# Optimization experiments

Measured on AMD Instinct MI355X. Metric: run time of the kernel, lower is better.

Reference implementation:

```python
import jax, jax.numpy as jnp
import numpy as np

B, T, D, H = 32, 2048, 512, 512


def setup_inputs() -> dict:
    key = jax.random.key(0)
    k1, k2 = jax.random.split(key)
    x = jax.random.normal(k1, (B, T, D), dtype=jnp.float32)
    # Linear(D+H -> 4H); xavier-uniform-ish init
    limit = float(np.sqrt(6.0 / ((D + H) + 4 * H)))
    W = jax.random.uniform(k2, (D + H, 4 * H), minval=-limit, maxval=limit, dtype=jnp.float32)
    b = jnp.zeros((4 * H,), dtype=jnp.float32)
    b = b.at[H:2 * H].set(1.0)  # forget-gate bias init = 1
    h0 = jnp.zeros((B, H), dtype=jnp.float32)
    c0 = jnp.zeros((B, H), dtype=jnp.float32)
    return {"x": x, "W": W, "b": b, "h0": h0, "c0": c0}


def reference(x, W, b, h0, c0):
    # Split weight into input and hidden parts to avoid per-step concat.
    Wx, Wh = W[:D], W[D:]  # (D,4H), (H,4H)
    # Precompute input projections for all timesteps: (T,B,4H)
    xg = jnp.einsum('btd,dg->tbg', x, Wx) + b

    def step(carry, xg_t):
        h, c = carry
        gates = xg_t + h @ Wh  # (B,4H)
        i, f, g, o = jnp.split(gates, 4, axis=-1)
        i = jax.nn.sigmoid(i)
        f = jax.nn.sigmoid(f)
        g = jnp.tanh(g)
        o = jax.nn.sigmoid(o)
        c_t = f * c + i * g
        h_t = o * jnp.tanh(c_t)
        return (h_t, c_t), h_t

    (h_T, c_T), hs = jax.lax.scan(step, (h0, c0), xg)  # hs: (T,B,H)
    outputs = jnp.transpose(hs, (1, 0, 2))  # (B,T,H)
    return outputs, (h_T, c_T)
```

## Files before the change

### kernel.cpp

```cpp
#include <hip/hip_runtime.h>

#define TT 2048
#define BB 32
#define DD 512
#define HH 512
#define NWG 64
#define NTHR 256

typedef short s8v __attribute__((ext_vector_type(8)));
typedef float f4v __attribute__((ext_vector_type(4)));
typedef unsigned u4v __attribute__((ext_vector_type(4)));
typedef unsigned long long u64;

union UF { u4v u; s8v s; };

__device__ __forceinline__ float asf(unsigned u) { return __uint_as_float(u); }

__device__ __forceinline__ unsigned cvtpk(float a, float b) {
    unsigned r;
    asm("v_cvt_pk_bf16_f32 %0, %1, %2" : "=v"(r) : "v"(a), "v"(b));
    return r;
}
__device__ __forceinline__ void split2(float a, float b, unsigned& hp, unsigned& lp) {
    hp = cvtpk(a, b);
    lp = cvtpk(a - asf(hp << 16), b - asf(hp & 0xFFFF0000u));
}

__global__ void lstm_init(const float* __restrict__ h0, const float* __restrict__ c0,
                          unsigned* __restrict__ hhi, float* __restrict__ cbuf,
                          unsigned* __restrict__ flags) {
    int j = blockIdx.x * blockDim.x + threadIdx.x;
    if (j < NWG * 4) flags[j] = 0u;
    if (j < BB * HH / 2) hhi[j] = cvtpk(h0[2 * j], h0[2 * j + 1]);
    cbuf[j] = c0[j];
}

__global__ __launch_bounds__(NTHR) void gemm_xg(
    const float* __restrict__ x, const float* __restrict__ W,
    const float* __restrict__ bias, float* __restrict__ xg, int t0)
{
    const int wg8 = blockIdx.x & 63;
    const int tcb = blockIdx.x >> 6;
    const int tid = threadIdx.x;
    const int u0  = wg8 * 8;
    const int wv  = tid >> 6, ln = tid & 63;
    const int bh  = wv >> 1, ch = wv & 1;
    const int fl  = ln & 15, fg = ln >> 4;

    s8v whi[16], wlo[16];
    const int col32 = ch * 16 + fl;
    const int gcol  = ((col32 >> 3) << 9) + u0 + (col32 & 7);
    #pragma unroll
    for (int it = 0; it < 16; ++it) {
        float v[8];
        #pragma unroll
        for (int j = 0; j < 8; ++j)
            v[j] = W[(size_t)(it * 32 + fg * 8 + j) * 2048 + gcol];
        UF H, L;
        #pragma unroll
        for (int q = 0; q < 4; ++q) {
            unsigned hp, lp;
            split2(v[2 * q], v[2 * q + 1], hp, lp);
            H.u[q] = hp; L.u[q] = lp;
        }
        whi[it] = H.s; wlo[it] = L.s;
    }
    const float bcol = bias[gcol];

    const int arow = bh * 16 + fl;
    const float* xlane = x + (size_t)arow * TT * DD + fg * 8;
    const int crow = bh * 16 + fg * 4;

    for (int ii = 0; ii < 64; ++ii) {
        const int i = tcb * 64 + ii;
        const int t = t0 + i;
        f4v acc  = {0.f, 0.f, 0.f, 0.f};
        f4v accl = {0.f, 0.f, 0.f, 0.f};
        const float* xs = xlane + (size_t)t * DD;
        #pragma unroll
        for (int it = 0; it < 16; ++it) {
            float4 f0 = *(const float4*)(xs + it * 32);
            float4 f1 = *(const float4*)(xs + it * 32 + 4);
            UF H, L;
            unsigned hp, lp;
            split2(f0.x, f0.y, hp, lp); H.u[0] = hp; L.u[0] = lp;
            split2(f0.z, f0.w, hp, lp); H.u[1] = hp; L.u[1] = lp;
            split2(f1.x, f1.y, hp, lp); H.u[2] = hp; L.u[2] = lp;
            split2(f1.z, f1.w, hp, lp); H.u[3] = hp; L.u[3] = lp;
            acc  = __builtin_amdgcn_mfma_f32_16x16x32_bf16(H.s, whi[it], acc, 0, 0, 0);
            accl = __builtin_amdgcn_mfma_f32_16x16x32_bf16(L.s, whi[it], accl, 0, 0, 0);
            accl = __builtin_amdgcn_mfma_f32_16x16x32_bf16(H.s, wlo[it], accl, 0, 0, 0);
        }
        float4 st = {acc[0] + accl[0] + bcol, acc[1] + accl[1] + bcol,
                     acc[2] + accl[2] + bcol, acc[3] + accl[3] + bcol};
        *(float4*)(xg + (size_t)i * 65536 + (size_t)gcol * 32 + crow) = st;
    }
}

__global__ __launch_bounds__(NTHR, 1) void lstm_scan(
    const float* __restrict__ W,
    const float* __restrict__ xg,
    float* __restrict__ out,
    unsigned* hhi,
    float* __restrict__ cbuf,
    unsigned* flags, int t0, int nt)
{
    const int wg  = blockIdx.x;
    const int tid = threadIdx.x;
    const int u0  = wg * 8;
    const int wv  = tid >> 6, ln = tid & 63;
    const int bh  = wv >> 1;
    const int tile = wv & 1;
    const int lr  = ln & 15;
    const int lk  = ln >> 4;

    s8v whi[16];
    {
        const int wcol = (lr & 3) * 512 + u0 + tile * 4 + (lr >> 2);
        #pragma unroll
        for (int it = 0; it < 16; ++it) {
            UF H;
            #pragma unroll
            for (int q = 0; q < 4; ++q) {
                float a = W[(size_t)(512 + it * 32 + lk * 8 + 2 * q) * 2048 + wcol];
                float b = W[(size_t)(512 + it * 32 + lk * 8 + 2 * q + 1) * 2048 + wcol];
                H.u[q] = cvtpk(a, b);
            }
            whi[it] = H.s;
        }
    }

    const int batch = bh * 16 + lr;
    const int uglob = u0 + tile * 4 + lk;
    float cst = cbuf[batch * HH + uglob];

    const int hb = batch * 256;

    for (int i = 0; i < nt; ++i) {
        const int t = t0 + i;

        const float* xi = xg + (size_t)i * 65536;
        float xgi = xi[(size_t)(0 * 512 + uglob) * 32 + batch];
        float xgf = xi[(size_t)(1 * 512 + uglob) * 32 + batch];
        float xgg = xi[(size_t)(2 * 512 + uglob) * 32 + batch];
        float xgo = xi[(size_t)(3 * 512 + uglob) * 32 + batch];

        if (t > 0) {
            const u64* f64 = (const u64*)flags;
            for (;;) {
                u64 a = __hip_atomic_load(&f64[ln * 2], __ATOMIC_RELAXED,
                                          __HIP_MEMORY_SCOPE_AGENT);
                u64 b = __hip_atomic_load(&f64[ln * 2 + 1], __ATOMIC_RELAXED,
                                          __HIP_MEMORY_SCOPE_AGENT);
                unsigned m0 = min((unsigned)a, (unsigned)(a >> 32));
                unsigned m1 = min((unsigned)b, (unsigned)(b >> 32));
                if (__all(min(m0, m1) >= (unsigned)t)) break;
            }
            __builtin_amdgcn_fence(__ATOMIC_ACQUIRE, "agent");
        }

        f4v acc = {0.f, 0.f, 0.f, 0.f};
        {
            const unsigned* hh = hhi + (size_t)(t & 1) * (BB * HH / 2);
            #pragma unroll
            for (int it = 0; it < 16; ++it) {
                UF H;
                H.u = *(const u4v*)(hh + hb + it * 16 + lk * 4);
                acc = __builtin_amdgcn_mfma_f32_16x16x32_bf16(whi[it], H.s, acc, 0, 0, 0);
            }
        }

        float gi = xgi + acc[0];
        float gf = xgf + acc[1];
        float gg = xgg + acc[2];
        float go = xgo + acc[3];
        float si = 1.0f / (1.0f + __expf(-gi));
        float sf = 1.0f / (1.0f + __expf(-gf));
        float e2 = __expf(2.0f * fminf(fmaxf(gg, -15.f), 15.f));
        float tg = (e2 - 1.0f) / (e2 + 1.0f);
        float so = 1.0f / (1.0f + __expf(-go));
        cst = sf * cst + si * tg;
        float e2c = __expf(2.0f * fminf(fmaxf(cst, -15.f), 15.f));
        float h = so * (e2c - 1.0f) / (e2c + 1.0f);

        {
            float hn = __shfl_down(h, 16);
            if ((lk & 1) == 0) {
                unsigned hp = cvtpk(h, hn);
                unsigned* dh = hhi + (size_t)((t + 1) & 1) * (BB * HH / 2);
                __hip_atomic_store(&dh[batch * 256 + (uglob >> 1)], hp,
                                   __ATOMIC_RELAXED, __HIP_MEMORY_SCOPE_AGENT);
            }
        }
        asm volatile("s_waitcnt vmcnt(0)" ::: "memory");
        __builtin_amdgcn_sched_barrier(0);
        if (ln == 0)
            __hip_atomic_store(&flags[wg * 4 + wv], (unsigned)(t + 1),
                               __ATOMIC_RELAXED, __HIP_MEMORY_SCOPE_AGENT);

        out[(size_t)batch * TT * HH + (size_t)t * HH + uglob] = h;
        if (t == TT - 1) {
            size_t ho = (size_t)BB * TT * HH;
            out[ho + batch * HH + uglob] = h;
            out[ho + (size_t)BB * HH + batch * HH + uglob] = cst;
        }
    }

    cbuf[batch * HH + uglob] = cst;
}

extern "C" void kernel_launch(void* const* d_in, const int* in_sizes, int n_in,
                              void* d_out, int out_size, void* d_ws, size_t ws_size,
                              hipStream_t stream) {
    const float* x  = nullptr;
    const float* W  = nullptr;
    const float* b  = nullptr;
    const float* h0 = nullptr;
    const float* c0 = nullptr;
    for (int i = 0; i < n_in; ++i) {
        int sz = in_sizes[i];
        if      (sz == BB * TT * DD)       x = (const float*)d_in[i];
        else if (sz == (DD + HH) * 4 * HH) W = (const float*)d_in[i];
        else if (sz == 4 * HH)             b = (const float*)d_in[i];
        else if (sz == BB * HH) { if (!h0) h0 = (const float*)d_in[i];
                                  else     c0 = (const float*)d_in[i]; }
    }
    float* out = (float*)d_out;

    char* base = (char*)d_ws;
    unsigned* hhi   = (unsigned*)(base);
    float*    cbuf  = (float*)   (base + 65536);
    unsigned* flags = (unsigned*)(base + 131072);
    float*    xg    = (float*)   (base + 135168);

    size_t avail = (ws_size > 135168) ? ws_size - 135168 : 0;
    size_t maxT  = avail / (BB * 2048 * sizeof(float));
    int Tc = (int)((maxT / 64) * 64);
    if (Tc > TT) Tc = TT;
    if (Tc < 64) Tc = 64;

    lstm_init<<<64, NTHR, 0, stream>>>(h0, c0, hhi, cbuf, flags);

    for (int t0 = 0; t0 < TT; t0 += Tc) {
        int nt = (TT - t0 < Tc) ? (TT - t0) : Tc;
        gemm_xg<<<(nt / 64) * 64, NTHR, 0, stream>>>(x, W, b, xg, t0);
        lstm_scan<<<NWG, NTHR, 0, stream>>>(W, xg, out, hhi, cbuf, flags, t0, nt);
    }
}
```

Measured before the change: 20.17 ms.

## Replace flag-based step barrier with poison-marked triple-buffered hidden state

The scan kernel no longer publishes per-wave flags and spins on them. Consumers instead poll the hidden-state buffer directly until no word holds a NaN poison value, and triple buffering lets each step re-poison the slot that will be written next. This removes the flag store, its vmcnt wait on the critical path and the separate flag poll, so the h data itself carries readiness. The gemm_xg grid is also split four ways over time for more parallelism, and workspace chunking allows partial chunks. It relies on bf16 h never producing the exact poison pattern and on per-word store visibility.

After: 17.42 ms. -13.6%, faster.

```diff
diff --git a/kernel.cpp b/kernel.cpp
--- a/kernel.cpp
+++ b/kernel.cpp
@@ -6,11 +6,11 @@
 #define HH 512
 #define NWG 64
 #define NTHR 256
+#define POISON 0x7FC07FC0u
 
 typedef short s8v __attribute__((ext_vector_type(8)));
 typedef float f4v __attribute__((ext_vector_type(4)));
 typedef unsigned u4v __attribute__((ext_vector_type(4)));
-typedef unsigned long long u64;
 
 union UF { u4v u; s8v s; };
 
@@ -27,20 +27,23 @@
 }
 
 __global__ void lstm_init(const float* __restrict__ h0, const float* __restrict__ c0,
-                          unsigned* __restrict__ hhi, float* __restrict__ cbuf,
-                          unsigned* __restrict__ flags) {
+                          unsigned* __restrict__ hbuf, float* __restrict__ cbuf) {
     int j = blockIdx.x * blockDim.x + threadIdx.x;
-    if (j < NWG * 4) flags[j] = 0u;
-    if (j < BB * HH / 2) hhi[j] = cvtpk(h0[2 * j], h0[2 * j + 1]);
+    if (j < BB * HH / 2) {
+        hbuf[j] = cvtpk(h0[2 * j], h0[2 * j + 1]);
+        hbuf[8192 + j]  = POISON;
+        hbuf[16384 + j] = POISON;
+    }
     cbuf[j] = c0[j];
 }
 
 __global__ __launch_bounds__(NTHR) void gemm_xg(
     const float* __restrict__ x, const float* __restrict__ W,
-    const float* __restrict__ bias, float* __restrict__ xg, int t0)
+    const float* __restrict__ bias, float* __restrict__ xg, int t0, int nt)
 {
     const int wg8 = blockIdx.x & 63;
-    const int tcb = blockIdx.x >> 6;
+    const int tq  = (blockIdx.x >> 6) & 3;
+    const int tb  = blockIdx.x >> 8;
     const int tid = threadIdx.x;
     const int u0  = wg8 * 8;
     const int wv  = tid >> 6, ln = tid & 63;
@@ -71,8 +74,9 @@
     const float* xlane = x + (size_t)arow * TT * DD + fg * 8;
     const int crow = bh * 16 + fg * 4;
 
-    for (int ii = 0; ii < 64; ++ii) {
-        const int i = tcb * 64 + ii;
+    for (int ii = 0; ii < 16; ++ii) {
+        const int i = tb * 64 + tq * 16 + ii;
+        if (i >= nt) break;
         const int t = t0 + i;
         f4v acc  = {0.f, 0.f, 0.f, 0.f};
         f4v accl = {0.f, 0.f, 0.f, 0.f};
@@ -101,9 +105,9 @@
     const float* __restrict__ W,
     const float* __restrict__ xg,
     float* __restrict__ out,
-    unsigned* hhi,
+    unsigned* hbuf,
     float* __restrict__ cbuf,
-    unsigned* flags, int t0, int nt)
+    int t0, int nt)
 {
     const int wg  = blockIdx.x;
     const int tid = threadIdx.x;
@@ -134,10 +138,15 @@
     const int uglob = u0 + tile * 4 + lk;
     float cst = cbuf[batch * HH + uglob];
 
-    const int hb = batch * 256;
+    const int hb   = batch * 256;
+    const int slot = batch * 256 + (uglob >> 1);
+
+    int rot = t0 % 3;
 
     for (int i = 0; i < nt; ++i) {
         const int t = t0 + i;
+        const int rotP = (rot == 2) ? 0 : rot + 1;
+        const int rotZ = (rotP == 2) ? 0 : rotP + 1;
 
         const float* xi = xg + (size_t)i * 65536;
         float xgi = xi[(size_t)(0 * 512 + uglob) * 32 + batch];
@@ -145,29 +154,33 @@
         float xgg = xi[(size_t)(2 * 512 + uglob) * 32 + batch];
         float xgo = xi[(size_t)(3 * 512 + uglob) * 32 + batch];
 
-        if (t > 0) {
-            const u64* f64 = (const u64*)flags;
-            for (;;) {
-                u64 a = __hip_atomic_load(&f64[ln * 2], __ATOMIC_RELAXED,
-                                          __HIP_MEMORY_SCOPE_AGENT);
-                u64 b = __hip_atomic_load(&f64[ln * 2 + 1], __ATOMIC_RELAXED,
-                                          __HIP_MEMORY_SCOPE_AGENT);
-                unsigned m0 = min((unsigned)a, (unsigned)(a >> 32));
-                unsigned m1 = min((unsigned)b, (unsigned)(b >> 32));
-                if (__all(min(m0, m1) >= (unsigned)t)) break;
-            }
+        const unsigned* bufR = hbuf + (size_t)rot * 8192;
+        u4v f[16];
+        unsigned vm = 0;
+        do {
             __builtin_amdgcn_fence(__ATOMIC_ACQUIRE, "agent");
-        }
-
-        f4v acc = {0.f, 0.f, 0.f, 0.f};
-        {
-            const unsigned* hh = hhi + (size_t)(t & 1) * (BB * HH / 2);
             #pragma unroll
             for (int it = 0; it < 16; ++it) {
-                UF H;
-                H.u = *(const u4v*)(hh + hb + it * 16 + lk * 4);
-                acc = __builtin_amdgcn_mfma_f32_16x16x32_bf16(whi[it], H.s, acc, 0, 0, 0);
+                if (!(vm & (1u << it))) {
+                    u4v v = *(const u4v*)(bufR + hb + it * 16 + lk * 4);
+                    if (v[0] != POISON && v[1] != POISON &&
+                        v[2] != POISON && v[3] != POISON) {
+                        f[it] = v; vm |= 1u << it;
+                    }
+                }
             }
+        } while (vm != 0xFFFFu);
+
+        unsigned* bufZ = hbuf + (size_t)rotZ * 8192;
+        if ((lk & 1) == 0)
+            __hip_atomic_store(&bufZ[slot], POISON,
+                               __ATOMIC_RELAXED, __HIP_MEMORY_SCOPE_AGENT);
+
+        f4v acc = {0.f, 0.f, 0.f, 0.f};
+        #pragma unroll
+        for (int it = 0; it < 16; ++it) {
+            UF F; F.u = f[it];
+            acc = __builtin_amdgcn_mfma_f32_16x16x32_bf16(whi[it], F.s, acc, 0, 0, 0);
         }
 
         float gi = xgi + acc[0];
@@ -183,20 +196,17 @@
         float e2c = __expf(2.0f * fminf(fmaxf(cst, -15.f), 15.f));
         float h = so * (e2c - 1.0f) / (e2c + 1.0f);
 
+        asm volatile("s_waitcnt vmcnt(0)" ::: "memory");
+        __builtin_amdgcn_sched_barrier(0);
+
         {
             float hn = __shfl_down(h, 16);
             if ((lk & 1) == 0) {
-                unsigned hp = cvtpk(h, hn);
-                unsigned* dh = hhi + (size_t)((t + 1) & 1) * (BB * HH / 2);
-                __hip_atomic_store(&dh[batch * 256 + (uglob >> 1)], hp,
+                unsigned* bufP = hbuf + (size_t)rotP * 8192;
+                __hip_atomic_store(&bufP[slot], cvtpk(h, hn),
                                    __ATOMIC_RELAXED, __HIP_MEMORY_SCOPE_AGENT);
             }
         }
-        asm volatile("s_waitcnt vmcnt(0)" ::: "memory");
-        __builtin_amdgcn_sched_barrier(0);
-        if (ln == 0)
-            __hip_atomic_store(&flags[wg * 4 + wv], (unsigned)(t + 1),
-                               __ATOMIC_RELAXED, __HIP_MEMORY_SCOPE_AGENT);
 
         out[(size_t)batch * TT * HH + (size_t)t * HH + uglob] = h;
         if (t == TT - 1) {
@@ -204,6 +214,8 @@
             out[ho + batch * HH + uglob] = h;
             out[ho + (size_t)BB * HH + batch * HH + uglob] = cst;
         }
+
+        rot = rotP;
     }
 
     cbuf[batch * HH + uglob] = cst;
@@ -228,22 +240,21 @@
     float* out = (float*)d_out;
 
     char* base = (char*)d_ws;
-    unsigned* hhi   = (unsigned*)(base);
-    float*    cbuf  = (float*)   (base + 65536);
-    unsigned* flags = (unsigned*)(base + 131072);
-    float*    xg    = (float*)   (base + 135168);
-
-    size_t avail = (ws_size > 135168) ? ws_size - 135168 : 0;
-    size_t maxT  = avail / (BB * 2048 * sizeof(float));
-    int Tc = (int)((maxT / 64) * 64);
-    if (Tc > TT) Tc = TT;
-    if (Tc < 64) Tc = 64;
-
-    lstm_init<<<64, NTHR, 0, stream>>>(h0, c0, hhi, cbuf, flags);
+    unsigned* hbuf = (unsigned*)(base);
+    float*    cbuf = (float*)   (base + 98304);
+    float*    xg   = (float*)   (base + 163840);
+
+    size_t avail = (ws_size > 163840) ? ws_size - 163840 : 0;
+    long maxT = (long)(avail / 262144);
+    int Tc = (maxT > TT) ? TT : (int)maxT;
+    if (Tc < 32) Tc = 32;
+
+    lstm_init<<<64, NTHR, 0, stream>>>(h0, c0, hbuf, cbuf);
 
     for (int t0 = 0; t0 < TT; t0 += Tc) {
         int nt = (TT - t0 < Tc) ? (TT - t0) : Tc;
-        gemm_xg<<<(nt / 64) * 64, NTHR, 0, stream>>>(x, W, b, xg, t0);
-        lstm_scan<<<NWG, NTHR, 0, stream>>>(W, xg, out, hhi, cbuf, flags, t0, nt);
-    }
-}
+        int tblocks = (nt + 63) / 64;
+        gemm_xg<<<tblocks * 256, NTHR, 0, stream>>>(x, W, b, xg, t0, nt);
+        lstm_scan<<<NWG, NTHR, 0, stream>>>(W, xg, out, hbuf, cbuf, t0, nt);
+    }
+}
```
